# Optimization experiments

Measured on AMD Instinct MI355X. Metric: run time of the kernel, lower is better.

Reference implementation:

```python
import jax, jax.numpy as jnp
import numpy as np

B, S, K = 64, 512, 16
USERS, ITEMS = 100000, 100000
DU, DI = 64, 192
H = DU + DI  # 256, hidden_dim = user_dim + item_dim


def _layernorm(x, g, b):
    m = jnp.mean(x, -1, keepdims=True)
    v = jnp.var(x, -1, keepdims=True)
    return (x - m) / jnp.sqrt(v + 1e-5) * g + b


def setup_inputs() -> dict:
    key = jax.random.key(0)
    ks = jax.random.split(key, 40)
    g = lambda i, shape, s=0.02: jax.random.normal(ks[i], shape, jnp.float32) * s
    return dict(
        users=jax.random.randint(ks[0], (B,), 0, USERS),
        candidates=jax.random.randint(ks[1], (B, S), 0, ITEMS),
        targets_idx=jax.random.randint(ks[2], (B, K), 0, S),
        embed_user=g(3, (USERS, DU), 1.0),
        embed_item=g(4, (ITEMS, DI), 1.0),
        Wq=g(5, (H, H)), bq=jnp.zeros((H,), jnp.float32),
        Wk=g(6, (H, H)), bk=jnp.zeros((H,), jnp.float32),
        Wv=g(7, (H, H)), bv=jnp.zeros((H,), jnp.float32),
        Wo=g(8, (H, H)), bo=jnp.zeros((H,), jnp.float32),
        ln1_g=jnp.ones((H,), jnp.float32), ln1_b=jnp.zeros((H,), jnp.float32),
        Wf1=g(9, (H, 4 * H)), bf1=jnp.zeros((4 * H,), jnp.float32),
        Wf2=g(10, (4 * H, H)), bf2=jnp.zeros((H,), jnp.float32),
        ln2_g=jnp.ones((H,), jnp.float32), ln2_b=jnp.zeros((H,), jnp.float32),
        W_ih=g(11, (4 * H, H)), W_hh=g(12, (4 * H, H)),
        b_ih=jnp.zeros((4 * H,), jnp.float32), b_hh=jnp.zeros((4 * H,), jnp.float32),
        W_D1=g(13, (2 * H, H)), W_D2=g(14, (H, H)),
        bias1=jnp.zeros((H,), jnp.float32), V_D1=g(15, (H,)),
        W_D3=g(16, (3 * H, H)), W_D4=g(17, (H, H)),
        bias2=jnp.zeros((H,), jnp.float32), V_D2=g(18, (H,)),
    )


def reference(users, candidates, targets_idx, embed_user, embed_item,
              Wq, bq, Wk, bk, Wv, bv, Wo, bo, ln1_g, ln1_b,
              Wf1, bf1, Wf2, bf2, ln2_g, ln2_b,
              W_ih, W_hh, b_ih, b_hh,
              W_D1, W_D2, bias1, V_D1, W_D3, W_D4, bias2, V_D2):
    Bc, Sc = candidates.shape
    # encode: item||user embeddings -> 1-layer, 1-head transformer encoder
    ue = jnp.broadcast_to(embed_user[users][:, None, :], (Bc, Sc, DU))
    x = jnp.concatenate([embed_item[candidates], ue], -1)  # (B,S,H)
    q = x @ Wq + bq
    kk = x @ Wk + bk
    v = x @ Wv + bv
    att = jax.nn.softmax(jnp.einsum('bqh,bkh->bqk', q, kk) / jnp.sqrt(jnp.float32(H)), -1)
    x = _layernorm(x + jnp.einsum('bqk,bkh->bqh', att, v) @ Wo + bo, ln1_g, ln1_b)
    x = _layernorm(x + jax.nn.relu(x @ Wf1 + bf1) @ Wf2 + bf2, ln2_g, ln2_b)
    enc = x                                           # (B,S,H) candidates_embed
    enc_t = jnp.transpose(enc, (1, 0, 2))             # (S,B,H)
    # gather target embeddings; step 0 input is zeros (targets_embed[0] unused)
    tgt = jnp.take_along_axis(enc, targets_idx[..., None], axis=1)  # (B,K,H)
    inputs = jnp.transpose(tgt, (1, 0, 2)).at[0].set(0.0)           # (K,B,H)

    def cell(hc, xin):  # custom LSTMCell with packed (h,c) state of size 2H
        h, c = jnp.split(hc, 2, -1)
        gates = xin @ W_ih.T + b_ih + h @ W_hh.T + b_hh
        i_, f_, g_, o_ = jnp.split(gates, 4, -1)
        c = jax.nn.sigmoid(f_) * c + jax.nn.sigmoid(i_) * jnp.tanh(g_)
        h = jax.nn.sigmoid(o_) * jnp.tanh(c)
        hc = jnp.concatenate([h, c], -1)
        return hc, hc

    hc0 = jnp.zeros((Bc, 2 * H), x.dtype)
    _, dec = jax.lax.scan(cell, hc0, inputs)          # (K,B,2H)
    # glimpse attention (Bahdanau additive, softmax over enc axis=1)
    e = jnp.tanh((dec @ W_D1)[:, None] + (enc_t @ W_D2)[None] + bias1)  # (K,S,B,H)
    a = jax.nn.softmax(e @ V_D1, axis=1)              # (K,S,B)
    glim = jnp.einsum('ksb,sbh->kbh', a, enc_t)       # (K,B,H)
    gcat = jnp.concatenate([dec, glim], -1)           # (K,B,3H)
    # pointer attention -> raw logits (output_prob=False, no masks)
    e2 = jnp.tanh((gcat @ W_D3)[:, None] + (enc_t @ W_D4)[None] + bias2)  # (K,S,B,H)
    logits = e2 @ V_D2                                # (K,S,B)
    return jnp.transpose(logits, (2, 0, 1))           # (B,K,S)
```

## Files before the change

### kernel.cpp

```cpp
#include <hip/hip_runtime.h>
#include <hip/hip_bf16.h>
#include <math.h>

#define B_   64
#define S_   512
#define K_   16
#define H_   256
#define H4_  1024

typedef __attribute__((ext_vector_type(4))) float f32x4;
typedef __attribute__((ext_vector_type(8))) short bf16x8;

__device__ __forceinline__ float wave_reduce_sum(float v) {
#pragma unroll
  for (int off = 32; off; off >>= 1) v += __shfl_down(v, off, 64);
  return v;
}
__device__ __forceinline__ float wave_reduce_max(float v) {
#pragma unroll
  for (int off = 32; off; off >>= 1) v = fmaxf(v, __shfl_down(v, off, 64));
  return v;
}
__device__ __forceinline__ float tanh_fast(float x) {
  const float e = __expf(2.f * x);
  return 1.f - __fdividef(2.f, e + 1.f);
}
__device__ __forceinline__ float sigmoid_fast(float x) {
  return __fdividef(1.f, 1.f + __expf(-x));
}
__device__ __forceinline__ ushort f2bf(float f) {
  union { float f; unsigned u; } v; v.f = f;
  unsigned r = v.u + 0x7FFFu + ((v.u >> 16) & 1u);
  return (ushort)(r >> 16);
}

__global__ void gather_x(const int* __restrict__ users, const int* __restrict__ cand,
                         const float* __restrict__ eu, const float* __restrict__ ei,
                         float* __restrict__ x, ushort* __restrict__ xb)
{
  int idx = blockIdx.x * 256 + threadIdx.x;
  int h  = idx & (H_ - 1);
  int bs = idx >> 8;
  int b  = bs >> 9;
  float v;
  if (h < 192) v = ei[(long)cand[bs] * 192 + h];
  else         v = eu[(long)users[b] * 64 + (h - 192)];
  x[idx] = v;
  xb[idx] = f2bf(v);
}

__global__ __launch_bounds__(256) void tcvt(const float* __restrict__ in, ushort* __restrict__ out,
                                            int R, int C)
{
  __shared__ float t[32][33];
  const int c0 = blockIdx.x * 32, r0 = blockIdx.y * 32;
  const int tx = threadIdx.x & 31, ty = threadIdx.x >> 5;
#pragma unroll
  for (int i = 0; i < 4; ++i)
    t[ty + 8 * i][tx] = in[(long)(r0 + ty + 8 * i) * C + c0 + tx];
  __syncthreads();
#pragma unroll
  for (int i = 0; i < 4; ++i)
    out[(long)(c0 + ty + 8 * i) * R + r0 + tx] = f2bf(t[tx][ty + 8 * i]);
}

__global__ void cvtflat(const float* __restrict__ in, ushort* __restrict__ out)
{
  int idx = blockIdx.x * 256 + threadIdx.x;
  out[idx] = f2bf(in[idx]);
}

template<int OM, bool RELU>
__global__ __launch_bounds__(256) void gemm_bf16(
    const ushort* __restrict__ A, const ushort* __restrict__ BT,
    const float* __restrict__ bias, void* __restrict__ Cv,
    int K, int ldA, int ldB, int ldC, long sA, long sB, long sC)
{
  __shared__ ushort Al[128][40];
  __shared__ ushort Bl[128][40];
  const int bx = blockIdx.x, by = blockIdx.y, bz = blockIdx.z;
  A  += (long)bz * sA + (long)by * 128 * ldA;
  BT += (long)bz * sB + (long)bx * 128 * ldB;
  const int tid = threadIdx.x, lane = tid & 63, wave = tid >> 6;
  const int wr = wave >> 1, wc = wave & 1;
  const int fr = lane & 15, fq = lane >> 4;
  const int srow = tid & 127;
  const int scol = (tid >> 7) * 16;

  const f32x4 fzero = {0.f, 0.f, 0.f, 0.f};
  f32x4 acc[4][4];
#pragma unroll
  for (int i = 0; i < 4; ++i)
#pragma unroll
    for (int j = 0; j < 4; ++j) acc[i][j] = fzero;

  for (int k0 = 0; k0 < K; k0 += 32) {
    const ushort* ap = A  + (long)srow * ldA + k0 + scol;
    const ushort* bp = BT + (long)srow * ldB + k0 + scol;
    *(uint4*)&Al[srow][scol]     = *(const uint4*)(ap);
    *(uint4*)&Al[srow][scol + 8] = *(const uint4*)(ap + 8);
    *(uint4*)&Bl[srow][scol]     = *(const uint4*)(bp);
    *(uint4*)&Bl[srow][scol + 8] = *(const uint4*)(bp + 8);
    __syncthreads();
    bf16x8 af[4], bfr[4];
#pragma unroll
    for (int i = 0; i < 4; ++i) af[i]  = *(const bf16x8*)&Al[wr * 64 + i * 16 + fr][fq * 8];
#pragma unroll
    for (int j = 0; j < 4; ++j) bfr[j] = *(const bf16x8*)&Bl[wc * 64 + j * 16 + fr][fq * 8];
#pragma unroll
    for (int i = 0; i < 4; ++i)
#pragma unroll
      for (int j = 0; j < 4; ++j)
        acc[i][j] = __builtin_amdgcn_mfma_f32_16x16x32_bf16(af[i], bfr[j], acc[i][j], 0, 0, 0);
    __syncthreads();
  }

  const int rowb = by * 128 + wr * 64 + fq * 4;
  const int colb = bx * 128 + wc * 64 + fr;
#pragma unroll
  for (int j = 0; j < 4; ++j) {
    const int colg = colb + j * 16;
    const float bb = bias ? bias[colg] : 0.f;
#pragma unroll
    for (int i = 0; i < 4; ++i) {
      const int rowg = rowb + i * 16;
      if (OM == 0) {
        float* C = (float*)Cv;
#pragma unroll
        for (int r = 0; r < 4; ++r) {
          float o = acc[i][j][r] + bb;
          if (RELU) o = fmaxf(o, 0.f);
          C[(long)bz * sC + (long)(rowg + r) * ldC + colg] = o;
        }
      } else if (OM == 1) {
        ushort* C = (ushort*)Cv;
#pragma unroll
        for (int r = 0; r < 4; ++r) {
          float o = acc[i][j][r] + bb;
          if (RELU) o = fmaxf(o, 0.f);
          C[(long)bz * sC + (long)(rowg + r) * ldC + colg] = f2bf(o);
        }
      } else if (OM == 2) {
        float* C = (float*)Cv;
        const long ct = ((long)(rowg >> 9) * H_ + colg) * S_ + (rowg & 511);
        float4 o;
        o.x = acc[i][j][0] + bb; o.y = acc[i][j][1] + bb;
        o.z = acc[i][j][2] + bb; o.w = acc[i][j][3] + bb;
        *(float4*)&C[ct] = o;
      } else {
        ushort* C = (ushort*)Cv;
        const long ct = ((long)(rowg >> 9) * H_ + colg) * S_ + (rowg & 511);
        ushort4 o;
        o.x = f2bf(acc[i][j][0] + bb); o.y = f2bf(acc[i][j][1] + bb);
        o.z = f2bf(acc[i][j][2] + bb); o.w = f2bf(acc[i][j][3] + bb);
        *(ushort4*)&C[ct] = o;
      }
    }
  }
}

__global__ __launch_bounds__(256) void attn_softmax(const float* __restrict__ att,
                                                    ushort* __restrict__ attb)
{
  __shared__ float red[4];
  const long row = blockIdx.x;
  const float* p = att + row * S_;
  const int t = threadIdx.x, lane = t & 63, wid = t >> 6;
  float v0 = p[t] * 0.0625f, v1 = p[t + 256] * 0.0625f;
  float m = wave_reduce_max(fmaxf(v0, v1));
  if (!lane) red[wid] = m;
  __syncthreads();
  const float bm = fmaxf(fmaxf(red[0], red[1]), fmaxf(red[2], red[3]));
  const float e0 = __expf(v0 - bm), e1 = __expf(v1 - bm);
  float s = wave_reduce_sum(e0 + e1);
  __syncthreads();
  if (!lane) red[wid] = s;
  __syncthreads();
  const float inv = __fdividef(1.f, red[0] + red[1] + red[2] + red[3]);
  ushort* q = attb + row * S_;
  q[t] = f2bf(e0 * inv); q[t + 256] = f2bf(e1 * inv);
}

__global__ __launch_bounds__(256) void ln_res(float* __restrict__ x, const float* __restrict__ y,
                                              const float* __restrict__ g, const float* __restrict__ b,
                                              ushort* __restrict__ xb)
{
  __shared__ float red[4];
  const long row = blockIdx.x;
  const int t = threadIdx.x, lane = t & 63, wid = t >> 6;
  float v = x[row * H_ + t] + y[row * H_ + t];
  float s = wave_reduce_sum(v);
  if (!lane) red[wid] = s;
  __syncthreads();
  const float mean = (red[0] + red[1] + red[2] + red[3]) * (1.f / H_);
  const float d = v - mean;
  float s2 = wave_reduce_sum(d * d);
  __syncthreads();
  if (!lane) red[wid] = s2;
  __syncthreads();
  const float var = (red[0] + red[1] + red[2] + red[3]) * (1.f / H_);
  const float o = d * rsqrtf(var + 1e-5f) * g[t] + b[t];
  x[row * H_ + t] = o;
  xb[row * H_ + t] = f2bf(o);
}

__global__ void gather_inputs(const int* __restrict__ tidx, const ushort* __restrict__ encb,
                              ushort* __restrict__ inpb)
{
  int idx = blockIdx.x * 256 + threadIdx.x;
  int h = idx & 255, kb = idx >> 8;
  int b = kb & 63, k = kb >> 6;
  ushort v = 0;
  if (k > 0) {
    int s = tidx[b * K_ + k];
    v = encb[((long)b * S_ + s) * H_ + h];
  }
  inpb[idx] = v;
}

__global__ void transpose_whh(const float* __restrict__ W, float* __restrict__ WT)
{
  int idx = blockIdx.x * 256 + threadIdx.x;
  int r = idx >> 8, d = idx & 255;
  WT[d * H4_ + r] = W[idx];
}

__global__ __launch_bounds__(1024) void lstm_all(const float* __restrict__ Xp,
                                                 const float* __restrict__ WhhT,
                                                 const float* __restrict__ b_hh,
                                                 float* __restrict__ dec)
{
  __shared__ float hs[H_];
  __shared__ float gates[H4_];
  const int b = blockIdx.x, j = threadIdx.x;
  float c = 0.f;
  if (j < H_) hs[j] = 0.f;
  const float bh = b_hh[j];
  __syncthreads();
  for (int step = 0; step < K_; ++step) {
    float acc = Xp[((long)step * B_ + b) * H4_ + j] + bh;
#pragma unroll 8
    for (int d = 0; d < H_; ++d)
      acc += hs[d] * WhhT[d * H4_ + j];
    gates[j] = acc;
    __syncthreads();
    if (j < H_) {
      const float gi = gates[j], gf = gates[256 + j], gg = gates[512 + j], go = gates[768 + j];
      c = sigmoid_fast(gf) * c + sigmoid_fast(gi) * tanh_fast(gg);
      const float h = sigmoid_fast(go) * tanh_fast(c);
      hs[j] = h;
      const long rw = ((long)step * B_ + b) * (2 * H_);
      dec[rw + j] = h;
      dec[rw + H_ + j] = c;
    }
    __syncthreads();
  }
}

__global__ __launch_bounds__(256) void glimpse_kernel(
    const float* __restrict__ decW1, const float* __restrict__ encW2T,
    const float* __restrict__ enc, const float* __restrict__ bias1,
    const float* __restrict__ V1, float* __restrict__ glim)
{
  __shared__ float dv[H_], vd[H_], sc[S_], red[4];
  const int bid = blockIdx.x;
  const int b = bid & 63;
  const int t = threadIdx.x, lane = t & 63, wv = t >> 6;
  dv[t] = decW1[(long)bid * H_ + t] + bias1[t];
  vd[t] = V1[t];
  __syncthreads();
  const float* ebase = encW2T + (long)b * H_ * S_;
  float a0 = 0.f, a1 = 0.f;
#pragma unroll 4
  for (int h = 0; h < H_; ++h) {
    const float d = dv[h], w = vd[h];
    const float* r = ebase + (long)h * S_;
    a0 += tanh_fast(d + r[t]) * w;
    a1 += tanh_fast(d + r[t + 256]) * w;
  }
  float m = wave_reduce_max(fmaxf(a0, a1));
  if (!lane) red[wv] = m;
  __syncthreads();
  const float bm = fmaxf(fmaxf(red[0], red[1]), fmaxf(red[2], red[3]));
  const float e0 = __expf(a0 - bm), e1 = __expf(a1 - bm);
  float ssum = wave_reduce_sum(e0 + e1);
  __syncthreads();
  if (!lane) red[wv] = ssum;
  __syncthreads();
  const float inv = __fdividef(1.f, red[0] + red[1] + red[2] + red[3]);
  sc[t] = e0 * inv; sc[t + 256] = e1 * inv;
  __syncthreads();
  float acc = 0.f;
  const float* eb = enc + (long)b * S_ * H_ + t;
#pragma unroll 4
  for (int s = 0; s < S_; ++s) acc += sc[s] * eb[(long)s * H_];
  glim[(long)bid * H_ + t] = acc;
}

__global__ void concat_gcat(const float* __restrict__ dec, const float* __restrict__ glim,
                            ushort* __restrict__ gcatb)
{
  int idx = blockIdx.x * 256 + threadIdx.x;
  int j = idx % 768, row = idx / 768;
  float v = (j < 512) ? dec[(long)row * 512 + j] : glim[(long)row * 256 + (j - 512)];
  gcatb[idx] = f2bf(v);
}

__global__ __launch_bounds__(256) void pointer_kernel(
    const float* __restrict__ gW3, const float* __restrict__ encW4T,
    const float* __restrict__ bias2, const float* __restrict__ V2,
    float* __restrict__ out)
{
  __shared__ float dv[H_], vd[H_];
  const int bid = blockIdx.x;
  const int b = bid & 63, k = bid >> 6;
  const int t = threadIdx.x;
  dv[t] = gW3[(long)bid * H_ + t] + bias2[t];
  vd[t] = V2[t];
  __syncthreads();
  const float* ebase = encW4T + (long)b * H_ * S_;
  float a0 = 0.f, a1 = 0.f;
#pragma unroll 4
  for (int h = 0; h < H_; ++h) {
    const float d = dv[h], w = vd[h];
    const float* r = ebase + (long)h * S_;
    a0 += tanh_fast(d + r[t]) * w;
    a1 += tanh_fast(d + r[t + 256]) * w;
  }
  const long ro = ((long)b * K_ + k) * S_;
  out[ro + t] = a0;
  out[ro + 256 + t] = a1;
}

extern "C" void kernel_launch(void* const* d_in, const int* in_sizes, int n_in,
                              void* d_out, int out_size, void* d_ws, size_t ws_size,
                              hipStream_t stream)
{
  const int*   users = (const int*)d_in[0];
  const int*   cand  = (const int*)d_in[1];
  const int*   tidx  = (const int*)d_in[2];
  const float* eu    = (const float*)d_in[3];
  const float* ei    = (const float*)d_in[4];
  const float* Wq    = (const float*)d_in[5];
  const float* bq    = (const float*)d_in[6];
  const float* Wk    = (const float*)d_in[7];
  const float* bk    = (const float*)d_in[8];
  const float* Wv    = (const float*)d_in[9];
  const float* bv    = (const float*)d_in[10];
  const float* Wo    = (const float*)d_in[11];
  const float* bo    = (const float*)d_in[12];
  const float* ln1g  = (const float*)d_in[13];
  const float* ln1b  = (const float*)d_in[14];
  const float* Wf1   = (const float*)d_in[15];
  const float* bf1   = (const float*)d_in[16];
  const float* Wf2   = (const float*)d_in[17];
  const float* bf2   = (const float*)d_in[18];
  const float* ln2g  = (const float*)d_in[19];
  const float* ln2b  = (const float*)d_in[20];
  const float* W_ih  = (const float*)d_in[21];
  const float* W_hh  = (const float*)d_in[22];
  const float* b_ih  = (const float*)d_in[23];
  const float* b_hh  = (const float*)d_in[24];
  const float* W_D1  = (const float*)d_in[25];
  const float* W_D2  = (const float*)d_in[26];
  const float* bias1 = (const float*)d_in[27];
  const float* V_D1  = (const float*)d_in[28];
  const float* W_D3  = (const float*)d_in[29];
  const float* W_D4  = (const float*)d_in[30];
  const float* bias2 = (const float*)d_in[31];
  const float* V_D2  = (const float*)d_in[32];

  float* ws = (float*)d_ws;
  float*  x      = ws;
  ushort* xb     = (ushort*)(ws + 8388608);
  ushort* qb     = (ushort*)(ws + 12582912);
  ushort* kb     = (ushort*)(ws + 16777216);
  ushort* vTb    = (ushort*)(ws + 20971520);
  ushort* aob    = (ushort*)(ws + 25165824);
  ushort* attb   = (ushort*)(ws + 29360128);
  float*  ych    = ws + 31457280;
  ushort* wts    = (ushort*)(ws + 33554432);
  float*  att    = ws + 34603008;
  ushort* midb   = (ushort*)att;
  float*  sm     = ws + 38797312;
  float*  encW2T = ws + 12582912;
  float*  encW4T = ws + 20971520;

  ushort* WqT  = wts;
  ushort* WkT  = WqT  + 65536;
  ushort* WvT  = WkT  + 65536;
  ushort* WoT  = WvT  + 65536;
  ushort* Wf1T = WoT  + 65536;
  ushort* Wf2T = Wf1T + 262144;
  ushort* WD1T = Wf2T + 262144;
  ushort* WD2T = WD1T + 131072;
  ushort* WD3T = WD2T + 65536;
  ushort* WD4T = WD3T + 196608;
  ushort* Wihb = WD4T + 65536;

  ushort* inpb   = (ushort*)sm;
  float*  Xp     = sm + 131072;
  float*  WhhT   = sm + 1179648;
  float*  dec    = sm + 1441792;
  ushort* decb   = (ushort*)(sm + 1966080);
  float*  decW1  = sm + 2228224;
  float*  glim   = sm + 2490368;
  ushort* gcatb  = (ushort*)(sm + 2752512);
  float*  gcatW3 = sm + 3145728;

  float* out = (float*)d_out;
  const long SH = (long)S_ * H_;

  tcvt<<<dim3(8,8),   dim3(256), 0, stream>>>(Wq,   WqT,  256, 256);
  tcvt<<<dim3(8,8),   dim3(256), 0, stream>>>(Wk,   WkT,  256, 256);
  tcvt<<<dim3(8,8),   dim3(256), 0, stream>>>(Wv,   WvT,  256, 256);
  tcvt<<<dim3(8,8),   dim3(256), 0, stream>>>(Wo,   WoT,  256, 256);
  tcvt<<<dim3(32,8),  dim3(256), 0, stream>>>(Wf1,  Wf1T, 256, 1024);
  tcvt<<<dim3(8,32),  dim3(256), 0, stream>>>(Wf2,  Wf2T, 1024, 256);
  tcvt<<<dim3(8,16),  dim3(256), 0, stream>>>(W_D1, WD1T, 512, 256);
  tcvt<<<dim3(8,8),   dim3(256), 0, stream>>>(W_D2, WD2T, 256, 256);
  tcvt<<<dim3(8,24),  dim3(256), 0, stream>>>(W_D3, WD3T, 768, 256);
  tcvt<<<dim3(8,8),   dim3(256), 0, stream>>>(W_D4, WD4T, 256, 256);
  cvtflat<<<dim3(1024), dim3(256), 0, stream>>>(W_ih, Wihb);

  gather_x<<<dim3(32768), dim3(256), 0, stream>>>(users, cand, eu, ei, x, xb);

  gemm_bf16<1,false><<<dim3(2,256), dim3(256), 0, stream>>>(xb, WqT, bq, qb,  256, 256, 256, 256, 0,0,0);
  gemm_bf16<1,false><<<dim3(2,256), dim3(256), 0, stream>>>(xb, WkT, bk, kb,  256, 256, 256, 256, 0,0,0);
  gemm_bf16<3,false><<<dim3(2,256), dim3(256), 0, stream>>>(xb, WvT, bv, vTb, 256, 256, 256, 0,   0,0,0);

  for (int c = 0; c < 4; ++c) {
    const long qo = (long)c * 16 * SH;
    gemm_bf16<0,false><<<dim3(4,4,16), dim3(256), 0, stream>>>(
        qb + qo, kb + qo, nullptr, att, 256, 256, 256, 512, SH, SH, (long)S_*S_);
    attn_softmax<<<dim3(16*S_), dim3(256), 0, stream>>>(att, attb);
    gemm_bf16<1,false><<<dim3(2,4,16), dim3(256), 0, stream>>>(
        attb, vTb + qo, nullptr, aob + qo, 512, 512, 512, 256, (long)S_*S_, SH, SH);
  }

  for (int c = 0; c < 4; ++c) {
    const long off = (long)c * 8192 * H_;
    gemm_bf16<0,false><<<dim3(2,64), dim3(256), 0, stream>>>(aob + off, WoT, bo, ych, 256, 256, 256, 256, 0,0,0);
    ln_res<<<dim3(8192), dim3(256), 0, stream>>>(x + off, ych, ln1g, ln1b, xb + off);
  }

  for (int c = 0; c < 4; ++c) {
    const long off = (long)c * 8192 * H_;
    gemm_bf16<1,true ><<<dim3(8,64), dim3(256), 0, stream>>>(xb + off, Wf1T, bf1, midb, 256, 256, 256, 1024, 0,0,0);
    gemm_bf16<0,false><<<dim3(2,64), dim3(256), 0, stream>>>(midb, Wf2T, bf2, ych, 1024, 1024, 1024, 256, 0,0,0);
    ln_res<<<dim3(8192), dim3(256), 0, stream>>>(x + off, ych, ln2g, ln2b, xb + off);
  }

  gemm_bf16<2,false><<<dim3(2,256), dim3(256), 0, stream>>>(xb, WD2T, nullptr, encW2T, 256, 256, 256, 0, 0,0,0);
  gemm_bf16<2,false><<<dim3(2,256), dim3(256), 0, stream>>>(xb, WD4T, nullptr, encW4T, 256, 256, 256, 0, 0,0,0);

  gather_inputs<<<dim3(1024), dim3(256), 0, stream>>>(tidx, xb, inpb);
  gemm_bf16<0,false><<<dim3(8,8), dim3(256), 0, stream>>>(inpb, Wihb, b_ih, Xp, 256, 256, 256, 1024, 0,0,0);
  transpose_whh<<<dim3(1024), dim3(256), 0, stream>>>(W_hh, WhhT);
  lstm_all<<<dim3(B_), dim3(1024), 0, stream>>>(Xp, WhhT, b_hh, dec);

  cvtflat<<<dim3(2048), dim3(256), 0, stream>>>(dec, decb);
  gemm_bf16<0,false><<<dim3(2,8), dim3(256), 0, stream>>>(decb, WD1T, nullptr, decW1, 512, 512, 512, 256, 0,0,0);
  glimpse_kernel<<<dim3(K_*B_), dim3(256), 0, stream>>>(decW1, encW2T, x, bias1, V_D1, glim);

  concat_gcat<<<dim3(3072), dim3(256), 0, stream>>>(dec, glim, gcatb);
  gemm_bf16<0,false><<<dim3(2,8), dim3(256), 0, stream>>>(gcatb, WD3T, nullptr, gcatW3, 768, 768, 768, 256, 0,0,0);
  pointer_kernel<<<dim3(K_*B_), dim3(256), 0, stream>>>(gcatW3, encW4T, bias2, V_D2, out);
}
```

Measured before the change: 1.186 ms.

## Run LSTM recurrence on bf16 MFMA and batch small weight conversions

Replaces the scalar fp32 LSTM recurrent matvec (1024 threads per batch row, each doing a 256-long dot product) with a 256-thread kernel that uses 16x16x32 bf16 MFMA on a bf16 copy of W_hh, keeping h in shared memory as bf16. Only row 0 of each MFMA tile is used, since h is broadcast across all A rows. The gate bias and input projection are added in the elementwise phase, and the separate W_hh transpose kernel becomes a flat bf16 conversion. Six 256x256 weight transposes are merged into one launch to cut launch overhead. The recurrent state now goes through bf16, which adds rounding error across the 16 steps.

```diff
diff --git a/kernel.cpp b/kernel.cpp
--- a/kernel.cpp
+++ b/kernel.cpp
@@ -62,6 +62,35 @@
 #pragma unroll
   for (int i = 0; i < 4; ++i)
     out[(long)(c0 + ty + 8 * i) * R + r0 + tx] = f2bf(t[tx][ty + 8 * i]);
+}
+
+__global__ __launch_bounds__(256) void tcvt6(
+    const float* __restrict__ i0, ushort* __restrict__ o0,
+    const float* __restrict__ i1, ushort* __restrict__ o1,
+    const float* __restrict__ i2, ushort* __restrict__ o2,
+    const float* __restrict__ i3, ushort* __restrict__ o3,
+    const float* __restrict__ i4, ushort* __restrict__ o4,
+    const float* __restrict__ i5, ushort* __restrict__ o5)
+{
+  __shared__ float t[32][33];
+  const float* in; ushort* out;
+  switch (blockIdx.z) {
+    case 0: in = i0; out = o0; break;
+    case 1: in = i1; out = o1; break;
+    case 2: in = i2; out = o2; break;
+    case 3: in = i3; out = o3; break;
+    case 4: in = i4; out = o4; break;
+    default: in = i5; out = o5; break;
+  }
+  const int c0 = blockIdx.x * 32, r0 = blockIdx.y * 32;
+  const int tx = threadIdx.x & 31, ty = threadIdx.x >> 5;
+#pragma unroll
+  for (int i = 0; i < 4; ++i)
+    t[ty + 8 * i][tx] = in[(long)(r0 + ty + 8 * i) * 256 + c0 + tx];
+  __syncthreads();
+#pragma unroll
+  for (int i = 0; i < 4; ++i)
+    out[(long)(c0 + ty + 8 * i) * 256 + r0 + tx] = f2bf(t[tx][ty + 8 * i]);
 }
 
 __global__ void cvtflat(const float* __restrict__ in, ushort* __restrict__ out)
@@ -218,40 +247,51 @@
   inpb[idx] = v;
 }
 
-__global__ void transpose_whh(const float* __restrict__ W, float* __restrict__ WT)
-{
-  int idx = blockIdx.x * 256 + threadIdx.x;
-  int r = idx >> 8, d = idx & 255;
-  WT[d * H4_ + r] = W[idx];
-}
-
-__global__ __launch_bounds__(1024) void lstm_all(const float* __restrict__ Xp,
-                                                 const float* __restrict__ WhhT,
+__global__ __launch_bounds__(256) void lstm_mfma(const float* __restrict__ Xp,
+                                                 const ushort* __restrict__ Whhb,
                                                  const float* __restrict__ b_hh,
                                                  float* __restrict__ dec)
 {
-  __shared__ float hs[H_];
+  __shared__ ushort hsb[H_];
   __shared__ float gates[H4_];
-  const int b = blockIdx.x, j = threadIdx.x;
+  const int b = blockIdx.x, tid = threadIdx.x;
+  const int lane = tid & 63, wave = tid >> 6;
+  const int fr = lane & 15, fq = lane >> 4;
+  const int n0 = wave * 256;
+  if (tid < 128) ((uint*)hsb)[tid] = 0;
   float c = 0.f;
-  if (j < H_) hs[j] = 0.f;
-  const float bh = b_hh[j];
+  const int j = tid;
+  const float bh0 = b_hh[j], bh1 = b_hh[256 + j], bh2 = b_hh[512 + j], bh3 = b_hh[768 + j];
   __syncthreads();
   for (int step = 0; step < K_; ++step) {
-    float acc = Xp[((long)step * B_ + b) * H4_ + j] + bh;
-#pragma unroll 8
-    for (int d = 0; d < H_; ++d)
-      acc += hs[d] * WhhT[d * H4_ + j];
-    gates[j] = acc;
+    bf16x8 af[8];
+#pragma unroll
+    for (int kc = 0; kc < 8; ++kc)
+      af[kc] = *(const bf16x8*)&hsb[kc * 32 + fq * 8];
+#pragma unroll 4
+    for (int nt = 0; nt < 16; ++nt) {
+      const ushort* wp = Whhb + (long)(n0 + nt * 16 + fr) * 256 + fq * 8;
+      f32x4 acc = {0.f, 0.f, 0.f, 0.f};
+#pragma unroll
+      for (int kc = 0; kc < 8; ++kc) {
+        const bf16x8 bf = *(const bf16x8*)(wp + kc * 32);
+        acc = __builtin_amdgcn_mfma_f32_16x16x32_bf16(af[kc], bf, acc, 0, 0, 0);
+      }
+      if (lane < 16) gates[n0 + nt * 16 + lane] = acc[0];
+    }
     __syncthreads();
-    if (j < H_) {
-      const float gi = gates[j], gf = gates[256 + j], gg = gates[512 + j], go = gates[768 + j];
+    {
+      const long xrow = ((long)step * B_ + b) * H4_ + j;
+      const float gi = gates[j]       + Xp[xrow]       + bh0;
+      const float gf = gates[256 + j] + Xp[xrow + 256] + bh1;
+      const float gg = gates[512 + j] + Xp[xrow + 512] + bh2;
+      const float go = gates[768 + j] + Xp[xrow + 768] + bh3;
       c = sigmoid_fast(gf) * c + sigmoid_fast(gi) * tanh_fast(gg);
       const float h = sigmoid_fast(go) * tanh_fast(c);
-      hs[j] = h;
       const long rw = ((long)step * B_ + b) * (2 * H_);
       dec[rw + j] = h;
       dec[rw + H_ + j] = c;
+      hsb[j] = f2bf(h);
     }
     __syncthreads();
   }
@@ -400,7 +440,7 @@
 
   ushort* inpb   = (ushort*)sm;
   float*  Xp     = sm + 131072;
-  float*  WhhT   = sm + 1179648;
+  ushort* Whhb   = (ushort*)(sm + 1179648);
   float*  dec    = sm + 1441792;
   ushort* decb   = (ushort*)(sm + 1966080);
   float*  decW1  = sm + 2228224;
@@ -411,17 +451,14 @@
   float* out = (float*)d_out;
   const long SH = (long)S_ * H_;
 
-  tcvt<<<dim3(8,8),   dim3(256), 0, stream>>>(Wq,   WqT,  256, 256);
-  tcvt<<<dim3(8,8),   dim3(256), 0, stream>>>(Wk,   WkT,  256, 256);
-  tcvt<<<dim3(8,8),   dim3(256), 0, stream>>>(Wv,   WvT,  256, 256);
-  tcvt<<<dim3(8,8),   dim3(256), 0, stream>>>(Wo,   WoT,  256, 256);
+  tcvt6<<<dim3(8,8,6), dim3(256), 0, stream>>>(Wq, WqT, Wk, WkT, Wv, WvT,
+                                               Wo, WoT, W_D2, WD2T, W_D4, WD4T);
   tcvt<<<dim3(32,8),  dim3(256), 0, stream>>>(Wf1,  Wf1T, 256, 1024);
   tcvt<<<dim3(8,32),  dim3(256), 0, stream>>>(Wf2,  Wf2T, 1024, 256);
   tcvt<<<dim3(8,16),  dim3(256), 0, stream>>>(W_D1, WD1T, 512, 256);
-  tcvt<<<dim3(8,8),   dim3(256), 0, stream>>>(W_D2, WD2T, 256, 256);
   tcvt<<<dim3(8,24),  dim3(256), 0, stream>>>(W_D3, WD3T, 768, 256);
-  tcvt<<<dim3(8,8),   dim3(256), 0, stream>>>(W_D4, WD4T, 256, 256);
   cvtflat<<<dim3(1024), dim3(256), 0, stream>>>(W_ih, Wihb);
+  cvtflat<<<dim3(1024), dim3(256), 0, stream>>>(W_hh, Whhb);
 
   gather_x<<<dim3(32768), dim3(256), 0, stream>>>(users, cand, eu, ei, x, xb);
 
@@ -456,8 +493,7 @@
 
   gather_inputs<<<dim3(1024), dim3(256), 0, stream>>>(tidx, xb, inpb);
   gemm_bf16<0,false><<<dim3(8,8), dim3(256), 0, stream>>>(inpb, Wihb, b_ih, Xp, 256, 256, 256, 1024, 0,0,0);
-  transpose_whh<<<dim3(1024), dim3(256), 0, stream>>>(W_hh, WhhT);
-  lstm_all<<<dim3(B_), dim3(1024), 0, stream>>>(Xp, WhhT, b_hh, dec);
+  lstm_mfma<<<dim3(B_), dim3(256), 0, stream>>>(Xp, Whhb, b_hh, dec);
 
   cvtflat<<<dim3(2048), dim3(256), 0, stream>>>(dec, decb);
   gemm_bf16<0,false><<<dim3(2,8), dim3(256), 0, stream>>>(decb, WD1T, nullptr, decW1, 512, 512, 512, 256, 0,0,0);
```

Result: slower. 1.267 ms (+6.8%).
